# Kernel tuning notes

Measured on AMD Instinct MI355X. Metric: run time of the kernel, lower is better.

The kernel has to match this reference:

```python
import jax, jax.numpy as jnp
import numpy as np

B, A, C, H, W = 4, 6, 80, 128, 128
INPUT_SHIFT = 4
IMG = 1024.0
K_PRE = 4095            # kSRamSize: pre-NMS candidate budget
POST_K = 300            # post_nms_top_k
THR_INT = 1             # ceil(0.05 * 2**INPUT_SHIFT)
NMS_THR = 128.0 / 256.0 # ceil(0.5 * 2**kNmsThresholdShift) / 2**8
MARGIN_INT = 0          # ceil(0.0 * 2**INPUT_SHIFT)
CLASS_OFFSET = 0
NEG = -(1 << 30)
OUT_SHIFT = 2           # kOutputBBoxShift


def setup_inputs() -> dict:
    key = jax.random.key(0)
    k1, = jax.random.split(key, 1)
    # quantized int8 repr (scale 1/2**4) of box deltas + class scores
    data = jax.random.randint(k1, (B, A * (4 + C), H, W), -128, 128, dtype=jnp.int32)
    # grid anchors: centers at stride 8, per-anchor square sizes
    stride = IMG / H
    ys, xs = np.meshgrid(np.arange(H), np.arange(W), indexing="ij")
    cx = ((xs + 0.5) * stride).astype(np.float32)
    cy = ((ys + 0.5) * stride).astype(np.float32)
    half = (32.0 * (1.33 ** np.arange(A, dtype=np.float32)))[:, None, None] / 2.0
    anchor = np.stack([cx[None] - half, cy[None] - half, cx[None] + half, cy[None] + half], axis=1)
    # exp table exactly as _gen_exp_table with in_scale = 1/2**INPUT_SHIFT
    idx = np.arange(-128, 128, dtype=np.float32) / (1 << INPUT_SHIFT)
    ev = np.exp(idx)
    bit_num = float(np.ceil(np.log2(ev.max() + 1.0)))
    exp_shift = int(max(15 - bit_num, INPUT_SHIFT))
    exp_table = np.round(ev * (1 << exp_shift)).astype(np.int32)
    return {"data": data, "anchor": jnp.asarray(anchor, jnp.float32),
            "exp_table": jnp.asarray(exp_table), "exp_shift": exp_shift}


def _decode(data, anchor, exp_table, exp_shift):
    d = data.reshape(B, A, 4 + C, H, W)
    deltas = jnp.transpose(d[:, :, :4], (0, 1, 3, 4, 2)).reshape(B, -1, 4)   # [B,N,4] int
    cls = jnp.transpose(d[:, :, 4:], (0, 1, 3, 4, 2)).reshape(B, -1, C)      # [B,N,C] int
    score = cls.max(-1)                                   # int, scale 1/2**4
    label = jnp.argmax(cls, -1).astype(jnp.int32) + CLASS_OFFSET
    anc = jnp.transpose(anchor, (0, 2, 3, 1)).reshape(-1, 4)                 # [N,4] matches (A,H,W)
    aw = anc[:, 2] - anc[:, 0]
    ah = anc[:, 3] - anc[:, 1]
    acx = (anc[:, 0] + anc[:, 2]) * 0.5
    acy = (anc[:, 1] + anc[:, 3]) * 0.5
    inv = 1.0 / (1 << INPUT_SHIFT)
    dx = deltas[..., 0].astype(jnp.float32) * inv
    dy = deltas[..., 1].astype(jnp.float32) * inv
    esc = 1.0 / (1 << exp_shift)
    ew = exp_table[jnp.clip(deltas[..., 2], -128, 127) + 128].astype(jnp.float32) * esc
    eh = exp_table[jnp.clip(deltas[..., 3], -128, 127) + 128].astype(jnp.float32) * esc
    pcx = acx + dx * aw
    pcy = acy + dy * ah
    pw = aw * ew
    ph = ah * eh
    boxes = jnp.stack([pcx - pw * 0.5, pcy - ph * 0.5, pcx + pw * 0.5, pcy + ph * 0.5], -1)
    return jnp.clip(boxes, 0.0, IMG), score, label       # use_clippings


def _iou(b):  # [K,4] -> [K,K]
    area = jnp.maximum(b[:, 2] - b[:, 0], 0.0) * jnp.maximum(b[:, 3] - b[:, 1], 0.0)
    lt = jnp.maximum(b[:, None, :2], b[None, :, :2])
    rb = jnp.minimum(b[:, None, 2:], b[None, :, 2:])
    wh = jnp.maximum(rb - lt, 0.0)
    inter = wh[..., 0] * wh[..., 1]
    return inter / jnp.maximum(area[:, None] + area[None, :] - inter, 1e-6)


def _nms(boxes, scores, labels):
    # boxes/scores are pre-sorted by descending score
    sup = (_iou(boxes) > NMS_THR) \
          & (labels[:, None] == labels[None, :]) \
          & ((scores[:, None] - scores[None, :]) >= MARGIN_INT)
    valid = scores > NEG
    idx = jnp.arange(K_PRE)

    def body(i, keep):
        sup_i = sup[i] & (idx > i)
        return jnp.where(keep[i] & valid[i], keep & jnp.logical_not(sup_i), keep)

    return jax.lax.fori_loop(0, K_PRE, body, valid)


def reference(data, anchor, exp_table, exp_shift):
    boxes, score, label = _decode(data, anchor, exp_table, exp_shift)
    ms = jnp.where(score >= THR_INT, score, NEG)          # box_filter_threshold
    topv, topi = jax.lax.top_k(ms, K_PRE)                 # [B,K]
    boxes_k = jnp.take_along_axis(boxes, topi[:, :, None], axis=1)
    labels_k = jnp.take_along_axis(label, topi, axis=1)
    keep = jax.vmap(_nms)(boxes_k, topv, labels_k)
    fs = jnp.where(keep, topv, NEG)
    outv, outi = jax.lax.top_k(fs, POST_K)
    out_boxes = jnp.take_along_axis(boxes_k, outi[:, :, None], axis=1)
    out_labels = jnp.take_along_axis(labels_k, outi, axis=1)
    out_boxes_i = jnp.round(out_boxes * (1 << OUT_SHIFT)).astype(jnp.int32)  # qint16 @ kOutputBBoxShift
    return out_boxes_i, outv.astype(jnp.int32), out_labels
```

## Files before the change

### kernel.cpp

```cpp
#include <hip/hip_runtime.h>
#include <stdint.h>

#define BATCH 4
#define NA 6
#define NC 80
#define HW (128*128)
#define NPB (NA*HW)
#define KPRE 4095
#define KPAD 4096
#define POSTK 300
#define NEGV (-(1<<30))
#define NCHUNK (NPB/256)

#define OFF_BOXES    0
#define OFF_BOXK     6291456
#define OFF_MS       6553600
#define OFF_LAB      8126464
#define OFF_BCNT     9699328
#define OFF_BASE     10485760
#define OFF_SCUT     10487808
#define OFF_TOPV     10487872
#define OFF_LABK     10553408
#define OFF_MASK     10618944

__global__ __launch_bounds__(256) void dpp_init_kernel(int* __restrict__ topv,
                                                       int* __restrict__ labk,
                                                       float4* __restrict__ boxk) {
    int i = blockIdx.x * 256 + threadIdx.x;
    topv[i] = NEGV;
    labk[i] = 0;
    boxk[i] = make_float4(0.f, 0.f, 0.f, 0.f);
}

__device__ __forceinline__ float4 dpp_decode_box(int dxi, int dyi, int dwi, int dhi,
                                                 float a0, float a1, float a2, float a3,
                                                 const int* __restrict__ exp_table, float esc) {
#pragma clang fp contract(off)
    float aw  = a2 - a0;
    float ah  = a3 - a1;
    float acx = (a0 + a2) * 0.5f;
    float acy = (a1 + a3) * 0.5f;
    float dx  = (float)dxi * 0.0625f;
    float dy  = (float)dyi * 0.0625f;
    int e2 = dwi < -128 ? -128 : (dwi > 127 ? 127 : dwi);
    int e3 = dhi < -128 ? -128 : (dhi > 127 ? 127 : dhi);
    float ew = (float)exp_table[e2 + 128] * esc;
    float eh = (float)exp_table[e3 + 128] * esc;
    float pcx = acx + dx * aw;
    float pcy = acy + dy * ah;
    float pw = aw * ew;
    float ph = ah * eh;
    float x0 = pcx - pw * 0.5f;
    float y0 = pcy - ph * 0.5f;
    float x1 = pcx + pw * 0.5f;
    float y1 = pcy + ph * 0.5f;
    x0 = fminf(fmaxf(x0, 0.f), 1024.f);
    y0 = fminf(fmaxf(y0, 0.f), 1024.f);
    x1 = fminf(fmaxf(x1, 0.f), 1024.f);
    y1 = fminf(fmaxf(y1, 0.f), 1024.f);
    return make_float4(x0, y0, x1, y1);
}

__global__ __launch_bounds__(256) void dpp_decode_kernel(
        const int* __restrict__ data, const float* __restrict__ anchor,
        const int* __restrict__ exp_table, const int* __restrict__ exp_shift_p,
        int* __restrict__ ms, int* __restrict__ labels, float4* __restrict__ boxes,
        int* __restrict__ blockcnt) {
    int b = blockIdx.z, a = blockIdx.y, tid = threadIdx.x;
    int idx = blockIdx.x * 256 + tid;
    const int2* dptr = (const int2*)(data + (size_t)(b * NA + a) * 84 * HW);

    int2 d0 = dptr[idx];
    int2 d1 = dptr[8192 + idx];
    int2 d2 = dptr[2 * 8192 + idx];
    int2 d3 = dptr[3 * 8192 + idx];

    int2 m = dptr[4 * 8192 + idx];
    int l0 = 0, l1 = 0;
#pragma unroll 8
    for (int c = 1; c < NC; c++) {
        int2 v = dptr[(4 + c) * 8192 + idx];
        if (v.x > m.x) { m.x = v.x; l0 = c; }
        if (v.y > m.y) { m.y = v.y; l1 = c; }
    }

    const float2* aptr = (const float2*)(anchor + (size_t)a * 4 * HW);
    float2 ax0 = aptr[idx];
    float2 ay0 = aptr[8192 + idx];
    float2 ax1 = aptr[2 * 8192 + idx];
    float2 ay1 = aptr[3 * 8192 + idx];

    int eshift = exp_shift_p[0];
    float esc = 1.0f / (float)(1 << eshift);

    float4 box0 = dpp_decode_box(d0.x, d1.x, d2.x, d3.x, ax0.x, ay0.x, ax1.x, ay1.x, exp_table, esc);
    float4 box1 = dpp_decode_box(d0.y, d1.y, d2.y, d3.y, ax0.y, ay0.y, ax1.y, ay1.y, exp_table, esc);

    int ms0 = (m.x >= 1) ? m.x : NEGV;
    int ms1 = (m.y >= 1) ? m.y : NEGV;

    size_t nb = (size_t)b * NPB + (size_t)a * HW;
    ((int2*)ms)[(nb >> 1) + idx] = make_int2(ms0, ms1);
    ((int2*)labels)[(nb >> 1) + idx] = make_int2(l0, l1);
    boxes[nb + 2 * (size_t)idx]     = box0;
    boxes[nb + 2 * (size_t)idx + 1] = box1;

    __shared__ int hist[256];
    hist[tid] = 0;
    __syncthreads();
    int half = tid >> 7;
    if (ms0 >= 1) atomicAdd(&hist[half * 128 + ms0], 1);
    if (ms1 >= 1) atomicAdd(&hist[half * 128 + ms1], 1);
    __syncthreads();
    int v = tid & 127, h2 = tid >> 7;
    int chunk = a * 64 + blockIdx.x * 2 + h2;
    blockcnt[((b << 7) + v) * NCHUNK + chunk] = hist[h2 * 128 + v];
}

__global__ __launch_bounds__(512) void dpp_cutoff_kernel(int* __restrict__ blockcnt,
                                                         int* __restrict__ base,
                                                         int* __restrict__ s_cut) {
    int t = threadIdx.x;
    int b = t >> 7, v = t & 127;
    __shared__ int tot[512];
    __shared__ int sc_lds[BATCH];
    int* bc = blockcnt + ((b << 7) + v) * NCHUNK;
    int sum = 0;
    for (int c = 0; c < NCHUNK; c++) sum += bc[c];
    tot[t] = sum;
    __syncthreads();
    if (v == 0) {
        int cum = 0, sc = 1;
        for (int vv = 127; vv >= 1; vv--) {
            base[(b << 7) + vv] = cum;
            cum += tot[(b << 7) + vv];
            sc = vv;
            if (cum >= KPRE) break;
        }
        sc_lds[b] = sc;
        s_cut[b] = sc;
    }
    __syncthreads();
    if (v >= 1 && v >= sc_lds[b]) {
        int run = 0;
        for (int c = 0; c < NCHUNK; c++) { int x = bc[c]; bc[c] = run; run += x; }
    }
}

__global__ __launch_bounds__(256) void dpp_place_kernel(
        const int* __restrict__ ms, const int* __restrict__ labels, const float4* __restrict__ boxes,
        const int* __restrict__ blockoff, const int* __restrict__ base, const int* __restrict__ s_cut,
        int* __restrict__ topv, int* __restrict__ labk, float4* __restrict__ boxk) {
    int chunk = blockIdx.x, b = blockIdx.y, tid = threadIdx.x;
    int n = (chunk << 8) + tid;
    int s = ms[(size_t)b * NPB + n];
    __shared__ int lds_s[256];
    lds_s[tid] = s;
    __syncthreads();
    int sc = s_cut[b];
    if (s >= sc) {
        int r = 0;
#pragma unroll 4
        for (int j = 0; j < tid; j++) r += (lds_s[j] == s) ? 1 : 0;
        int pos = base[(b << 7) + s] + blockoff[((b << 7) + s) * NCHUNK + chunk] + r;
        if (pos < KPRE) {
            topv[(b << 12) + pos] = s;
            labk[(b << 12) + pos] = labels[(size_t)b * NPB + n];
            boxk[(b << 12) + pos] = boxes[(size_t)b * NPB + n];
        }
    }
}

__global__ __launch_bounds__(64) void dpp_mask_kernel(
        const float4* __restrict__ boxk, const int* __restrict__ labk,
        unsigned long long* __restrict__ mask) {
#pragma clang fp contract(off)
    int cc = blockIdx.x, rc = blockIdx.y, b = blockIdx.z;
    int t = threadIdx.x;
    int row = (rc << 6) + t;
    if (cc < rc) {
        mask[((size_t)(b << 12) + row) * 64 + cc] = 0ull;
        return;
    }
    __shared__ float4 cb[64];
    __shared__ int cl[64];
    int col0 = cc << 6;
    cb[t] = boxk[(b << 12) + col0 + t];
    cl[t] = labk[(b << 12) + col0 + t];
    __syncthreads();
    float4 rbx = boxk[(b << 12) + row];
    int rl = labk[(b << 12) + row];
    float rw = fmaxf(rbx.z - rbx.x, 0.f), rh = fmaxf(rbx.w - rbx.y, 0.f);
    float ra = rw * rh;
    unsigned long long bits = 0ull;
#pragma unroll 4
    for (int j = 0; j < 64; j++) {
        float4 c = cb[j];
        float cw = fmaxf(c.z - c.x, 0.f), ch = fmaxf(c.w - c.y, 0.f);
        float ca = cw * ch;
        float lx = fmaxf(rbx.x, c.x), ly = fmaxf(rbx.y, c.y);
        float rx = fminf(rbx.z, c.z), ry = fminf(rbx.w, c.w);
        float wx = fmaxf(rx - lx, 0.f), wy = fmaxf(ry - ly, 0.f);
        float inter = wx * wy;
        float uni = fmaxf((ra + ca) - inter, 1e-6f);
        float iou = inter / uni;
        bool sup = (iou > 0.5f) && (cl[j] == rl) && ((col0 + j) > row);
        if (sup) bits |= (1ull << j);
    }
    mask[((size_t)(b << 12) + row) * 64 + cc] = bits;
}

__global__ __launch_bounds__(64) void dpp_nms_kernel(
        const float4* __restrict__ boxk, const int* __restrict__ labk, const int* __restrict__ topv,
        const unsigned long long* __restrict__ mask, int* __restrict__ out) {
    int b = blockIdx.x, lane = threadIdx.x;
    const int* tv = topv + (b << 12);
    const unsigned long long* mrow = mask + (size_t)(b << 12) * 64;

    unsigned long long sup = 0ull;
    for (int k = 0; k < 64; k++) {
        int v = tv[(k << 6) + lane];
        unsigned long long mb = __ballot(v <= NEGV);
        if (lane == k) sup = mb;
    }

    __shared__ int keep_lds[POSTK];
    int kc = 0;
    unsigned long long w_win = __shfl(sup, 0);

    unsigned long long pl[8], pu[8];
#pragma unroll
    for (int u = 0; u < 8; u++) {
        pl[u] = mrow[(size_t)u * 64 + lane];
        pu[u] = mrow[(size_t)u * 64 + 0];
    }

    bool done = false;
    for (int ii = 0; ii < KPAD && !done; ii += 8) {
#pragma unroll
        for (int u = 0; u < 8; u++) {
            int i = ii + u;
            if (!done && i < KPRE) {
                if ((i & 63) == 0 && i != 0) w_win = __shfl(sup, i >> 6);
                if (!((w_win >> (i & 63)) & 1ull)) {
                    if (lane == 0) keep_lds[kc] = i;
                    kc++;
                    if (kc == POSTK) {
                        done = true;
                    } else {
                        sup   |= pl[u];
                        w_win |= pu[u];
                    }
                }
            }
            int r = i + 8;
            if (r > KPRE - 1) r = KPRE - 1;
            pl[u] = mrow[(size_t)r * 64 + lane];
            pu[u] = mrow[(size_t)r * 64 + (r >> 6)];
        }
    }

    int kept = kc;
    if (kc < POSTK) {
        for (int j = 0; j < KPRE && kc < POSTK; j++) {
            unsigned long long w = __shfl(sup, j >> 6);
            if ((w >> (j & 63)) & 1ull) {
                if (lane == 0) keep_lds[kc] = j;
                kc++;
            }
        }
    }
    __syncthreads();

    for (int k = lane; k < POSTK; k += 64) {
        int slot = keep_lds[k];
        float4 bx = boxk[(b << 12) + slot];
        int lb = labk[(b << 12) + slot];
        int sv = (k < kept) ? tv[slot] : NEGV;
        int o = ((b * POSTK) + k) << 2;
        out[o + 0] = (int)rintf(bx.x * 4.0f);
        out[o + 1] = (int)rintf(bx.y * 4.0f);
        out[o + 2] = (int)rintf(bx.z * 4.0f);
        out[o + 3] = (int)rintf(bx.w * 4.0f);
        out[BATCH * POSTK * 4 + b * POSTK + k] = sv;
        out[BATCH * POSTK * 5 + b * POSTK + k] = lb;
    }
}

extern "C" void kernel_launch(void* const* d_in, const int* in_sizes, int n_in,
                              void* d_out, int out_size, void* d_ws, size_t ws_size,
                              hipStream_t stream) {
    const int*   data      = (const int*)d_in[0];
    const float* anchor    = (const float*)d_in[1];
    const int*   exp_table = (const int*)d_in[2];
    const int*   exp_shift = (const int*)d_in[3];

    char* ws = (char*)d_ws;
    float4* boxes  = (float4*)(ws + OFF_BOXES);
    float4* boxk   = (float4*)(ws + OFF_BOXK);
    int*    ms     = (int*)(ws + OFF_MS);
    int*    labels = (int*)(ws + OFF_LAB);
    int*    bcnt   = (int*)(ws + OFF_BCNT);
    int*    base   = (int*)(ws + OFF_BASE);
    int*    s_cut  = (int*)(ws + OFF_SCUT);
    int*    topv   = (int*)(ws + OFF_TOPV);
    int*    labk   = (int*)(ws + OFF_LABK);
    unsigned long long* mask = (unsigned long long*)(ws + OFF_MASK);

    dpp_init_kernel<<<64, 256, 0, stream>>>(topv, labk, boxk);
    dpp_decode_kernel<<<dim3(32, NA, BATCH), 256, 0, stream>>>(
        data, anchor, exp_table, exp_shift, ms, labels, boxes, bcnt);
    dpp_cutoff_kernel<<<1, 512, 0, stream>>>(bcnt, base, s_cut);
    dpp_place_kernel<<<dim3(NCHUNK, BATCH), 256, 0, stream>>>(
        ms, labels, boxes, bcnt, base, s_cut, topv, labk, boxk);
    dpp_mask_kernel<<<dim3(64, 64, BATCH), 64, 0, stream>>>(boxk, labk, mask);
    dpp_nms_kernel<<<BATCH, 64, 0, stream>>>(boxk, labk, topv, mask, (int*)d_out);
}
```

Baseline: 319.9 us.

## Parallelize per-bin chunk scan, widen decode vectors, merge init, batch mask rows

The serial per-thread loop over 384 chunks in the cutoff kernel becomes a new scan kernel with one block per (bin, batch) that does a wave-shuffle prefix sum and writes per-bin totals. The cutoff kernel then only reads those totals. Decode now handles four elements per thread with int4/float4 loads, and the init kernel is folded into the scan kernel. The mask kernel runs four 64-row tiles per 256-thread block so each column tile is loaded once per block instead of once per row tile. The scan now prefixes every bin, not just bins at or above the cutoff, which adds a little work in exchange for parallelism.

```diff
diff --git a/kernel.cpp b/kernel.cpp
--- a/kernel.cpp
+++ b/kernel.cpp
@@ -19,18 +19,10 @@
 #define OFF_BCNT     9699328
 #define OFF_BASE     10485760
 #define OFF_SCUT     10487808
-#define OFF_TOPV     10487872
-#define OFF_LABK     10553408
-#define OFF_MASK     10618944
-
-__global__ __launch_bounds__(256) void dpp_init_kernel(int* __restrict__ topv,
-                                                       int* __restrict__ labk,
-                                                       float4* __restrict__ boxk) {
-    int i = blockIdx.x * 256 + threadIdx.x;
-    topv[i] = NEGV;
-    labk[i] = 0;
-    boxk[i] = make_float4(0.f, 0.f, 0.f, 0.f);
-}
+#define OFF_TOT      10487872
+#define OFF_TOPV     10489920
+#define OFF_LABK     10555456
+#define OFF_MASK     10620992
 
 __device__ __forceinline__ float4 dpp_decode_box(int dxi, int dyi, int dwi, int dhi,
                                                  float a0, float a1, float a2, float a3,
@@ -68,82 +60,118 @@
         int* __restrict__ blockcnt) {
     int b = blockIdx.z, a = blockIdx.y, tid = threadIdx.x;
     int idx = blockIdx.x * 256 + tid;
-    const int2* dptr = (const int2*)(data + (size_t)(b * NA + a) * 84 * HW);
-
-    int2 d0 = dptr[idx];
-    int2 d1 = dptr[8192 + idx];
-    int2 d2 = dptr[2 * 8192 + idx];
-    int2 d3 = dptr[3 * 8192 + idx];
-
-    int2 m = dptr[4 * 8192 + idx];
-    int l0 = 0, l1 = 0;
-#pragma unroll 8
+    const int4* dptr = (const int4*)(data + (size_t)(b * NA + a) * 84 * HW);
+
+    int4 d0 = dptr[idx];
+    int4 d1 = dptr[4096 + idx];
+    int4 d2 = dptr[2 * 4096 + idx];
+    int4 d3 = dptr[3 * 4096 + idx];
+
+    int4 m = dptr[4 * 4096 + idx];
+    int4 lab = make_int4(0, 0, 0, 0);
+#pragma unroll 4
     for (int c = 1; c < NC; c++) {
-        int2 v = dptr[(4 + c) * 8192 + idx];
-        if (v.x > m.x) { m.x = v.x; l0 = c; }
-        if (v.y > m.y) { m.y = v.y; l1 = c; }
-    }
-
-    const float2* aptr = (const float2*)(anchor + (size_t)a * 4 * HW);
-    float2 ax0 = aptr[idx];
-    float2 ay0 = aptr[8192 + idx];
-    float2 ax1 = aptr[2 * 8192 + idx];
-    float2 ay1 = aptr[3 * 8192 + idx];
+        int4 v = dptr[(4 + c) * 4096 + idx];
+        if (v.x > m.x) { m.x = v.x; lab.x = c; }
+        if (v.y > m.y) { m.y = v.y; lab.y = c; }
+        if (v.z > m.z) { m.z = v.z; lab.z = c; }
+        if (v.w > m.w) { m.w = v.w; lab.w = c; }
+    }
+
+    const float4* aptr = (const float4*)(anchor + (size_t)a * 4 * HW);
+    float4 ax0 = aptr[idx];
+    float4 ay0 = aptr[4096 + idx];
+    float4 ax1 = aptr[2 * 4096 + idx];
+    float4 ay1 = aptr[3 * 4096 + idx];
 
     int eshift = exp_shift_p[0];
     float esc = 1.0f / (float)(1 << eshift);
 
     float4 box0 = dpp_decode_box(d0.x, d1.x, d2.x, d3.x, ax0.x, ay0.x, ax1.x, ay1.x, exp_table, esc);
     float4 box1 = dpp_decode_box(d0.y, d1.y, d2.y, d3.y, ax0.y, ay0.y, ax1.y, ay1.y, exp_table, esc);
-
-    int ms0 = (m.x >= 1) ? m.x : NEGV;
-    int ms1 = (m.y >= 1) ? m.y : NEGV;
+    float4 box2 = dpp_decode_box(d0.z, d1.z, d2.z, d3.z, ax0.z, ay0.z, ax1.z, ay1.z, exp_table, esc);
+    float4 box3 = dpp_decode_box(d0.w, d1.w, d2.w, d3.w, ax0.w, ay0.w, ax1.w, ay1.w, exp_table, esc);
+
+    int s0 = (m.x >= 1) ? m.x : NEGV;
+    int s1 = (m.y >= 1) ? m.y : NEGV;
+    int s2 = (m.z >= 1) ? m.z : NEGV;
+    int s3 = (m.w >= 1) ? m.w : NEGV;
 
     size_t nb = (size_t)b * NPB + (size_t)a * HW;
-    ((int2*)ms)[(nb >> 1) + idx] = make_int2(ms0, ms1);
-    ((int2*)labels)[(nb >> 1) + idx] = make_int2(l0, l1);
-    boxes[nb + 2 * (size_t)idx]     = box0;
-    boxes[nb + 2 * (size_t)idx + 1] = box1;
-
-    __shared__ int hist[256];
+    ((int4*)ms)[(nb >> 2) + idx] = make_int4(s0, s1, s2, s3);
+    ((int4*)labels)[(nb >> 2) + idx] = lab;
+    boxes[nb + 4 * (size_t)idx]     = box0;
+    boxes[nb + 4 * (size_t)idx + 1] = box1;
+    boxes[nb + 4 * (size_t)idx + 2] = box2;
+    boxes[nb + 4 * (size_t)idx + 3] = box3;
+
+    __shared__ int hist[512];
     hist[tid] = 0;
-    __syncthreads();
-    int half = tid >> 7;
-    if (ms0 >= 1) atomicAdd(&hist[half * 128 + ms0], 1);
-    if (ms1 >= 1) atomicAdd(&hist[half * 128 + ms1], 1);
-    __syncthreads();
-    int v = tid & 127, h2 = tid >> 7;
-    int chunk = a * 64 + blockIdx.x * 2 + h2;
-    blockcnt[((b << 7) + v) * NCHUNK + chunk] = hist[h2 * 128 + v];
-}
-
-__global__ __launch_bounds__(512) void dpp_cutoff_kernel(int* __restrict__ blockcnt,
+    hist[tid + 256] = 0;
+    __syncthreads();
+    int q = tid >> 6;
+    if (s0 >= 1) atomicAdd(&hist[q * 128 + s0], 1);
+    if (s1 >= 1) atomicAdd(&hist[q * 128 + s1], 1);
+    if (s2 >= 1) atomicAdd(&hist[q * 128 + s2], 1);
+    if (s3 >= 1) atomicAdd(&hist[q * 128 + s3], 1);
+    __syncthreads();
+#pragma unroll
+    for (int k = 0; k < 2; k++) {
+        int lin = tid + (k << 8);
+        int q2 = lin >> 7, v = lin & 127;
+        int chunk = a * 64 + blockIdx.x * 4 + q2;
+        blockcnt[((b << 7) + v) * NCHUNK + chunk] = hist[q2 * 128 + v];
+    }
+}
+
+__global__ __launch_bounds__(384) void dpp_scan_kernel(int* __restrict__ bcnt,
+                                                       int* __restrict__ tot,
+                                                       int* __restrict__ topv,
+                                                       int* __restrict__ labk,
+                                                       float4* __restrict__ boxk) {
+    int v = blockIdx.x, b = blockIdx.y, t = threadIdx.x;
+    if (t < 32) {
+        int slot = (b << 12) + (v << 5) + t;
+        topv[slot] = NEGV;
+        labk[slot] = 0;
+        boxk[slot] = make_float4(0.f, 0.f, 0.f, 0.f);
+    }
+    int* bc = bcnt + ((b << 7) + v) * NCHUNK;
+    int x = bc[t];
+    int lane = t & 63, w = t >> 6;
+    int s = x;
+#pragma unroll
+    for (int d = 1; d < 64; d <<= 1) {
+        int y = __shfl_up(s, d);
+        if (lane >= d) s += y;
+    }
+    __shared__ int wsum[6];
+    if (lane == 63) wsum[w] = s;
+    __syncthreads();
+    int off = 0;
+    for (int i = 0; i < w; i++) off += wsum[i];
+    int incl = s + off;
+    bc[t] = incl - x;
+    if (t == NCHUNK - 1) tot[(b << 7) + v] = incl;
+}
+
+__global__ __launch_bounds__(512) void dpp_cutoff_kernel(const int* __restrict__ tot,
                                                          int* __restrict__ base,
                                                          int* __restrict__ s_cut) {
     int t = threadIdx.x;
     int b = t >> 7, v = t & 127;
-    __shared__ int tot[512];
-    __shared__ int sc_lds[BATCH];
-    int* bc = blockcnt + ((b << 7) + v) * NCHUNK;
-    int sum = 0;
-    for (int c = 0; c < NCHUNK; c++) sum += bc[c];
-    tot[t] = sum;
+    __shared__ int lds[512];
+    lds[t] = tot[t];
     __syncthreads();
     if (v == 0) {
         int cum = 0, sc = 1;
         for (int vv = 127; vv >= 1; vv--) {
             base[(b << 7) + vv] = cum;
-            cum += tot[(b << 7) + vv];
+            cum += lds[(b << 7) + vv];
             sc = vv;
             if (cum >= KPRE) break;
         }
-        sc_lds[b] = sc;
         s_cut[b] = sc;
-    }
-    __syncthreads();
-    if (v >= 1 && v >= sc_lds[b]) {
-        int run = 0;
-        for (int c = 0; c < NCHUNK; c++) { int x = bc[c]; bc[c] = run; run += x; }
     }
 }
 
@@ -171,23 +199,27 @@
     }
 }
 
-__global__ __launch_bounds__(64) void dpp_mask_kernel(
+__global__ __launch_bounds__(256) void dpp_mask_kernel(
         const float4* __restrict__ boxk, const int* __restrict__ labk,
         unsigned long long* __restrict__ mask) {
 #pragma clang fp contract(off)
-    int cc = blockIdx.x, rc = blockIdx.y, b = blockIdx.z;
-    int t = threadIdx.x;
-    int row = (rc << 6) + t;
-    if (cc < rc) {
-        mask[((size_t)(b << 12) + row) * 64 + cc] = 0ull;
-        return;
-    }
+    int cc = blockIdx.x, rg = blockIdx.y, b = blockIdx.z;
+    int t = threadIdx.x, lane = t & 63;
+    int rc = (rg << 2) + (t >> 6);
+    int row = (rc << 6) + lane;
     __shared__ float4 cb[64];
     __shared__ int cl[64];
     int col0 = cc << 6;
-    cb[t] = boxk[(b << 12) + col0 + t];
-    cl[t] = labk[(b << 12) + col0 + t];
-    __syncthreads();
+    if (t < 64) {
+        cb[t] = boxk[(b << 12) + col0 + t];
+        cl[t] = labk[(b << 12) + col0 + t];
+    }
+    __syncthreads();
+    size_t mi = ((size_t)(b << 12) + row) * 64 + cc;
+    if (cc < rc) {
+        mask[mi] = 0ull;
+        return;
+    }
     float4 rbx = boxk[(b << 12) + row];
     int rl = labk[(b << 12) + row];
     float rw = fmaxf(rbx.z - rbx.x, 0.f), rh = fmaxf(rbx.w - rbx.y, 0.f);
@@ -207,7 +239,7 @@
         bool sup = (iou > 0.5f) && (cl[j] == rl) && ((col0 + j) > row);
         if (sup) bits |= (1ull << j);
     }
-    mask[((size_t)(b << 12) + row) * 64 + cc] = bits;
+    mask[mi] = bits;
 }
 
 __global__ __launch_bounds__(64) void dpp_nms_kernel(
@@ -303,16 +335,17 @@
     int*    bcnt   = (int*)(ws + OFF_BCNT);
     int*    base   = (int*)(ws + OFF_BASE);
     int*    s_cut  = (int*)(ws + OFF_SCUT);
+    int*    tot    = (int*)(ws + OFF_TOT);
     int*    topv   = (int*)(ws + OFF_TOPV);
     int*    labk   = (int*)(ws + OFF_LABK);
     unsigned long long* mask = (unsigned long long*)(ws + OFF_MASK);
 
-    dpp_init_kernel<<<64, 256, 0, stream>>>(topv, labk, boxk);
-    dpp_decode_kernel<<<dim3(32, NA, BATCH), 256, 0, stream>>>(
+    dpp_decode_kernel<<<dim3(16, NA, BATCH), 256, 0, stream>>>(
         data, anchor, exp_table, exp_shift, ms, labels, boxes, bcnt);
-    dpp_cutoff_kernel<<<1, 512, 0, stream>>>(bcnt, base, s_cut);
+    dpp_scan_kernel<<<dim3(128, BATCH), 384, 0, stream>>>(bcnt, tot, topv, labk, boxk);
+    dpp_cutoff_kernel<<<1, 512, 0, stream>>>(tot, base, s_cut);
     dpp_place_kernel<<<dim3(NCHUNK, BATCH), 256, 0, stream>>>(
         ms, labels, boxes, bcnt, base, s_cut, topv, labk, boxk);
-    dpp_mask_kernel<<<dim3(64, 64, BATCH), 64, 0, stream>>>(boxk, labk, mask);
+    dpp_mask_kernel<<<dim3(64, 16, BATCH), 256, 0, stream>>>(boxk, labk, mask);
     dpp_nms_kernel<<<BATCH, 64, 0, stream>>>(boxk, labk, topv, mask, (int*)d_out);
 }
```

Result: faster. 292.7 us (-8.5%).
